# Optimization experiments

Hardware: AMD Instinct MI355X
Metric: run time of the kernel (lower is better)

The kernel has to match this reference:

```python
import jax, jax.numpy as jnp
import numpy as np


def setup_inputs() -> dict:
    key = jax.random.key(0)
    ks = jax.random.split(key, 5)
    B, T, C = 2, 2048, 1024
    x = jax.random.normal(ks[0], (B, T, C), dtype=jnp.float32)
    Wqkv = jax.random.normal(ks[1], (C, 3 * C), dtype=jnp.float32) * (C ** -0.5)
    bqkv = jax.random.normal(ks[2], (3 * C,), dtype=jnp.float32) * 0.02
    Wproj = jax.random.normal(ks[3], (C, C), dtype=jnp.float32) * (C ** -0.5)
    bproj = jax.random.normal(ks[4], (C,), dtype=jnp.float32) * 0.02
    return {"x": x, "Wqkv": Wqkv, "bqkv": bqkv, "Wproj": Wproj, "bproj": bproj}


def reference(x, Wqkv, bqkv, Wproj, bproj):
    B, T, C = x.shape
    n_head = 16
    hd = C // n_head
    x_proj = x @ Wqkv + bqkv  # [B, T, 3C]
    # NOTE: source reshapes (B, T, C) -> (B, n_head, T, hd) directly (no transpose);
    # we replicate that exactly for faithfulness.
    q = x_proj[:, :, :C].reshape(B, n_head, T, hd)
    k = x_proj[:, :, C:2 * C].reshape(B, n_head, T, hd)
    v = x_proj[:, :, 2 * C:].reshape(B, n_head, T, hd)
    att = jnp.einsum('bhtd,bhsd->bhts', q, k) * (1.0 / jnp.sqrt(jnp.float32(hd)))
    causal = jnp.tril(jnp.ones((T, T), dtype=bool))  # True where allowed
    att = jnp.where(causal, att, jnp.float32(-jnp.inf))
    att = jax.nn.softmax(att, axis=-1)
    y = att @ v  # [B, H, T, hd]
    y = jnp.transpose(y, (0, 2, 1, 3)).reshape(B, T, C)
    return y @ Wproj + bproj
```

## Files before the change

### kernel.cpp

```cpp
#include <hip/hip_runtime.h>
#include <hip/hip_bf16.h>
#include <stdint.h>

typedef __hip_bfloat16 bf16;
typedef __attribute__((ext_vector_type(8))) short bf16x8;
typedef __attribute__((ext_vector_type(4))) float f32x4;

__device__ __forceinline__ bf16x8 ldsv8(const bf16* p) { return *(const bf16x8*)p; }

__device__ __forceinline__ short bf_bits(float f) {
  union { bf16 h; short s; } u; u.h = __float2bfloat16(f); return u.s;
}

#define QSCALE 0.18033688011112042f

#define ASYNC16(ldsdst, gsrc)                                                  \
  __builtin_amdgcn_global_load_lds(                                            \
      (const __attribute__((address_space(1))) void*)(gsrc),                   \
      (__attribute__((address_space(3))) void*)(ldsdst), 16, 0, 0)

__device__ __forceinline__ bool is_bf16(const void* p) {
  const uint32_t* w = (const uint32_t*)p;
  int cnt = 0;
#pragma unroll 8
  for (int i = 0; i < 64; ++i) {
    uint32_t e = (w[i] >> 7) & 0xffu;
    cnt += (e >= 100u && e <= 150u) ? 1 : 0;
  }
  return cnt >= 40;
}

__device__ __forceinline__ float load_f32(const void* p, size_t idx, bool b16) {
  return b16 ? __bfloat162float(((const bf16*)p)[idx]) : ((const float*)p)[idx];
}

__device__ __forceinline__ void cvtT_body(const void* in, bf16* out, int R,
                                          int Ccols, int bx, int by,
                                          bf16 (*tile)[33]) {
  const bool b16 = is_bf16(in);
  int tx = threadIdx.x & 31, ty = threadIdx.x >> 5;
  int c0 = bx * 32, r0 = by * 32;
#pragma unroll
  for (int i = 0; i < 32; i += 8)
    tile[ty + i][tx] = __float2bfloat16(load_f32(in, (size_t)(r0 + ty + i) * Ccols + c0 + tx, b16));
  __syncthreads();
#pragma unroll
  for (int i = 0; i < 32; i += 8)
    out[(size_t)(c0 + ty + i) * R + r0 + tx] = tile[tx][ty + i];
}

__global__ __launch_bounds__(256) void prep_k(const float* __restrict__ x,
                                              bf16* __restrict__ xb,
                                              const void* __restrict__ Wqkv,
                                              bf16* __restrict__ WqkvT,
                                              const void* __restrict__ Wproj,
                                              bf16* __restrict__ WprojT) {
  __shared__ __align__(16) bf16 tile[32][33];
  const int id = blockIdx.x;
  if (id < 2048) {
    size_t i = (size_t)id * 256 + threadIdx.x;
    const float4 f0 = ((const float4*)x)[i * 2];
    const float4 f1 = ((const float4*)x)[i * 2 + 1];
    bf16x8 pk = {bf_bits(f0.x), bf_bits(f0.y), bf_bits(f0.z), bf_bits(f0.w),
                 bf_bits(f1.x), bf_bits(f1.y), bf_bits(f1.z), bf_bits(f1.w)};
    ((bf16x8*)xb)[i] = pk;
  } else if (id < 5120) {
    int id2 = id - 2048;
    cvtT_body(Wqkv, WqkvT, 1024, 3072, id2 % 96, id2 / 96, tile);
  } else {
    int id3 = id - 5120;
    cvtT_body(Wproj, WprojT, 1024, 1024, id3 % 32, id3 / 32, tile);
  }
}

__global__ __launch_bounds__(256) void cvtT_k(const void* __restrict__ in,
                                              bf16* __restrict__ out,
                                              int R, int Ccols) {
  __shared__ __align__(16) bf16 tile[32][33];
  cvtT_body(in, out, R, Ccols, blockIdx.x, blockIdx.y, tile);
}

__global__ __launch_bounds__(256) void cvt_k(const float* __restrict__ in,
                                             bf16* __restrict__ out) {
  size_t i = (size_t)blockIdx.x * 256 + threadIdx.x;
  const float4 f0 = ((const float4*)in)[i * 2];
  const float4 f1 = ((const float4*)in)[i * 2 + 1];
  bf16x8 pk = {bf_bits(f0.x), bf_bits(f0.y), bf_bits(f0.z), bf_bits(f0.w),
               bf_bits(f1.x), bf_bits(f1.y), bf_bits(f1.z), bf_bits(f1.w)};
  ((bf16x8*)out)[i] = pk;
}

template <int MODE, int BN>
__global__ __launch_bounds__(256) void gemm128(
    const void* __restrict__ Araw, const bf16* __restrict__ BT,
    const void* __restrict__ biasraw, void* __restrict__ outv) {
  constexpr int K = 1024;
  constexpr int NBF = BN / 32;
  __shared__ __align__(16) bf16 As[128 * 32];
  __shared__ __align__(16) bf16 Bs[BN * 32];
  const int tid = threadIdx.x;
  const int wave = tid >> 6, lane = tid & 63;
  const int quad = lane >> 4, l16 = lane & 15;
  const int nwg = gridDim.x * gridDim.y;
  const int lin = blockIdx.y * gridDim.x + blockIdx.x;
  const int swz = (lin & 7) * (nwg >> 3) + (lin >> 3);
  const int m0 = (swz % gridDim.x) * 128, n0 = (swz / gridDim.x) * BN;
  const int wm = (wave & 1) * 64, wn = (wave >> 1) * (BN / 2);
  const bool a16 = (MODE == 0) ? is_bf16(Araw) : true;
  const bool bias16 = is_bf16(biasraw);

  f32x4 acc[4][NBF] = {};

  for (int kt = 0; kt < K; kt += 32) {
    __syncthreads();
    if (MODE != 0 || a16) {
#pragma unroll
      for (int i = 0; i < 2; ++i) {
        int slot = i * 256 + tid;
        int row = slot >> 2, col = (slot & 3) << 3;
        ASYNC16(As + slot * 8, ((const bf16*)Araw) + (size_t)(m0 + row) * K + kt + col);
      }
#pragma unroll
      for (int i = 0; i < BN / 64; ++i) {
        int slot = i * 256 + tid;
        int row = slot >> 2, col = (slot & 3) << 3;
        ASYNC16(Bs + slot * 8, BT + (size_t)(n0 + row) * K + kt + col);
      }
    } else {
#pragma unroll
      for (int i = 0; i < 2; ++i) {
        int slot = i * 256 + tid;
        int row = slot >> 2, col = (slot & 3) << 3;
        const float* ap = ((const float*)Araw) + (size_t)(m0 + row) * K + kt + col;
        float4 f0 = *(const float4*)ap;
        float4 f1 = *(const float4*)(ap + 4);
        bf16x8 pk = {bf_bits(f0.x), bf_bits(f0.y), bf_bits(f0.z), bf_bits(f0.w),
                     bf_bits(f1.x), bf_bits(f1.y), bf_bits(f1.z), bf_bits(f1.w)};
        *(bf16x8*)(As + slot * 8) = pk;
        if (i * 256 < BN * 4)
          *(bf16x8*)(Bs + slot * 8) = *(const bf16x8*)(BT + (size_t)(n0 + row) * K + kt + col);
      }
    }
    __syncthreads();
    bf16x8 af[4], bfr[NBF];
#pragma unroll
    for (int i = 0; i < 4; ++i)
      af[i] = ldsv8(As + (wm + i * 16 + l16) * 32 + quad * 8);
#pragma unroll
    for (int j = 0; j < NBF; ++j)
      bfr[j] = ldsv8(Bs + (wn + j * 16 + l16) * 32 + quad * 8);
#pragma unroll
    for (int i = 0; i < 4; ++i)
#pragma unroll
      for (int j = 0; j < NBF; ++j)
        acc[i][j] = __builtin_amdgcn_mfma_f32_16x16x32_bf16(af[i], bfr[j], acc[i][j], 0, 0, 0);
  }

  float biasf[NBF];
#pragma unroll
  for (int j = 0; j < NBF; ++j)
    biasf[j] = load_f32(biasraw, n0 + wn + j * 16 + l16, bias16);

#pragma unroll
  for (int i = 0; i < 4; ++i)
#pragma unroll
    for (int j = 0; j < NBF; ++j) {
      int ng = n0 + wn + j * 16 + l16;
#pragma unroll
      for (int r = 0; r < 4; ++r) {
        int mg = m0 + wm + i * 16 + quad * 4 + r;
        float v = acc[i][j][r] + biasf[j];
        if (MODE == 1) {
          ((float*)outv)[(size_t)mg * 1024 + ng] = v;
        } else {
          ((bf16*)outv)[(size_t)mg * 3072 + ng] =
              __float2bfloat16(ng < 1024 ? v * QSCALE : v);
        }
      }
    }
}

__global__ __launch_bounds__(1024, 4) void attn_k(const bf16* __restrict__ xproj,
                                                  bf16* __restrict__ Yb) {
  constexpr int KSZ = 128 * 72;
  constexpr int VSZ = 64 * 136;
  __shared__ __align__(16) bf16 Ks[2 * KSZ];
  __shared__ __align__(16) bf16 VTs[2 * VSZ];
  __shared__ __align__(16) bf16 Ps[16 * 16 * 136];

  const int tid = threadIdx.x;
  const int wave = tid >> 6, lane = tid & 63;
  const int quad = lane >> 4, l16 = lane & 15;
  const int tl = wave >> 3;
  const int wrow = (wave & 7) * 16;
  const int pid = blockIdx.x;
  const int qtA = pid, qtB = 15 - pid;
  const int qt = tl ? qtB : qtA;
  const int bh = blockIdx.y, b = bh >> 4, h = bh & 15;
  const size_t rowbase = (size_t)(b * 2048 + h * 128) * 3072;
  const int q0 = qt * 128;

  const short onebits = (short)0x3F80;
  const bf16x8 vones = {onebits, onebits, onebits, onebits,
                        onebits, onebits, onebits, onebits};

  bf16x8 aq[2];
  {
    int sg = q0 + wrow + l16;
    const bf16* qp = xproj + rowbase + (size_t)(sg >> 4) * 3072 + ((sg & 15) << 6);
#pragma unroll
    for (int ks = 0; ks < 2; ++ks)
      aq[ks] = *(const bf16x8*)(qp + ks * 32 + quad * 8);
  }

  f32x4 o[4] = {};
  f32x4 lacc = {};

  bf16* Pw = Ps + wave * (16 * 136);

  const int sA = tid >> 3, blkA = tid & 7;

  bf16x8 kreg, vreg;
#define ISSUE_LOADS(stv)                                                        \
  {                                                                             \
    int sg0 = (stv)*128 + sA;                                                   \
    const bf16* b0 = xproj + rowbase + (size_t)(sg0 >> 4) * 3072 + ((sg0 & 15) << 6); \
    kreg = *(const bf16x8*)(b0 + 1024 + blkA * 8);                              \
    vreg = *(const bf16x8*)(b0 + 2048 + blkA * 8);                              \
  }
#define WRITE_TILE(buf)                                                         \
  {                                                                             \
    bf16* Kd = Ks + (buf)*KSZ;                                                  \
    bf16* Vd = VTs + (buf)*VSZ;                                                 \
    *(bf16x8*)(Kd + sA * 72 + blkA * 8) = kreg;                                 \
    const bf16* ve0 = (const bf16*)&kreg;  (void)ve0;                           \
    const bf16* vv = (const bf16*)&vreg;                                        \
    const int ssw = sA ^ (blkA << 3);                                           \
    _Pragma("unroll")                                                           \
    for (int j = 0; j < 8; ++j) Vd[(blkA * 8 + j) * 136 + ssw] = vv[j];         \
  }

  ISSUE_LOADS(0);
  WRITE_TILE(0);
  ISSUE_LOADS(1);
  __syncthreads();

  int cur = 0;
  for (int st = 0; st <= qtB; ++st) {
    const bf16* Kc = Ks + cur * KSZ;
    const bf16* Vc = VTs + cur * VSZ;

    if (st <= qt) {
      const bool diag = (st == qt);

      f32x4 sc[8] = {};
      __builtin_amdgcn_s_setprio(1);
#pragma unroll
      for (int ks = 0; ks < 2; ++ks)
#pragma unroll
        for (int j = 0; j < 8; ++j) {
          bf16x8 bk = ldsv8(Kc + (j * 16 + l16) * 72 + (ks * 4 + quad) * 8);
          sc[j] = __builtin_amdgcn_mfma_f32_16x16x32_bf16(aq[ks], bk, sc[j], 0, 0, 0);
        }
      __builtin_amdgcn_s_setprio(0);

#pragma unroll
      for (int r = 0; r < 4; ++r) {
        const int rloc = wrow + quad * 4 + r;
        bf16* prow = Pw + (quad * 4 + r) * 136;
        const int psw = quad << 3;
#pragma unroll
        for (int j = 0; j < 8; ++j) {
          float v = sc[j][r];
          if (diag && (j * 16 + l16) > rloc) v = -1e30f;
          prow[(j * 16 + l16) ^ psw] = __float2bfloat16(__builtin_amdgcn_exp2f(v));
        }
      }

      __builtin_amdgcn_s_setprio(1);
#pragma unroll
      for (int ks = 0; ks < 4; ++ks) {
        bf16x8 ap = ldsv8(Pw + l16 * 136 + (((ks * 4 + quad) ^ (l16 >> 2)) << 3));
        lacc = __builtin_amdgcn_mfma_f32_16x16x32_bf16(ap, vones, lacc, 0, 0, 0);
#pragma unroll
        for (int j = 0; j < 4; ++j) {
          int d = j * 16 + l16;
          bf16x8 bv = ldsv8(Vc + d * 136 + (((ks * 4 + quad) ^ (2 * j + (l16 >> 3))) << 3));
          o[j] = __builtin_amdgcn_mfma_f32_16x16x32_bf16(ap, bv, o[j], 0, 0, 0);
        }
      }
      __builtin_amdgcn_s_setprio(0);
    }

    if (st < qtB) {
      WRITE_TILE(cur ^ 1);
      if (st + 2 <= qtB) ISSUE_LOADS(st + 2);
      __syncthreads();
      cur ^= 1;
    }
  }
#undef ISSUE_LOADS
#undef WRITE_TILE

  bf16* Yh = Yb + (size_t)b * 2097152 + h * 64;
#pragma unroll
  for (int r = 0; r < 4; ++r) {
    int tt = q0 + wrow + quad * 4 + r;
    float inv = 1.f / lacc[r];
#pragma unroll
    for (int j = 0; j < 4; ++j)
      Yh[(size_t)tt * 1024 + j * 16 + l16] = __float2bfloat16(o[j][r] * inv);
  }
}

extern "C" void kernel_launch(void* const* d_in, const int* in_sizes, int n_in,
                              void* d_out, int out_size, void* d_ws, size_t ws_size,
                              hipStream_t stream) {
  (void)out_size;
  const void* px     = d_in[0];
  const void* pWqkv  = (n_in > 1) ? d_in[1] : d_in[0];
  const void* pbqkv  = (n_in > 2) ? d_in[2] : d_in[0];
  const void* pWproj = (n_in > 3) ? d_in[3] : d_in[0];
  const void* pbproj = (n_in > 4) ? d_in[4] : d_in[0];
  for (int i = 0; i < n_in; ++i) {
    switch (in_sizes[i]) {
      case 4194304: px     = d_in[i]; break;
      case 3145728: pWqkv  = d_in[i]; break;
      case 3072:    pbqkv  = d_in[i]; break;
      case 1048576: pWproj = d_in[i]; break;
      case 1024:    pbproj = d_in[i]; break;
      default: break;
    }
  }

  char* ws = (char*)d_ws;
  bf16* xproj = (bf16*)(ws + 0);

  if (ws_size >= 41943040) {
    bf16* xb     = (bf16*)(ws + 25165824);
    bf16* WqkvT  = (bf16*)(ws + 33554432);
    bf16* WprojT = (bf16*)(ws + 39845888);
    bf16* Yb     = (bf16*)(ws + 27262976);

    prep_k<<<dim3(6144), 256, 0, stream>>>((const float*)px, xb, pWqkv, WqkvT,
                                           pWproj, WprojT);
    gemm128<0, 128><<<dim3(32, 24), 256, 0, stream>>>(xb, WqkvT, pbqkv, xproj);
    attn_k<<<dim3(8, 32), 1024, 0, stream>>>(xproj, Yb);
    gemm128<1, 64><<<dim3(32, 16), 256, 0, stream>>>(Yb, WprojT, pbproj, d_out);
  } else if (ws_size >= 39845888) {
    bf16* xb     = (bf16*)(ws + 25165824);
    bf16* WqkvT  = (bf16*)(ws + 33554432);
    bf16* WprojT = (bf16*)(ws + 25165824);
    bf16* Yb     = (bf16*)(ws + 27262976);

    cvt_k<<<dim3(2048), 256, 0, stream>>>((const float*)px, xb);
    cvtT_k<<<dim3(96, 32), 256, 0, stream>>>(pWqkv, WqkvT, 1024, 3072);
    gemm128<0, 128><<<dim3(32, 24), 256, 0, stream>>>(xb, WqkvT, pbqkv, xproj);
    cvtT_k<<<dim3(32, 32), 256, 0, stream>>>(pWproj, WprojT, 1024, 1024);
    attn_k<<<dim3(8, 32), 1024, 0, stream>>>(xproj, Yb);
    gemm128<1, 64><<<dim3(32, 16), 256, 0, stream>>>(Yb, WprojT, pbproj, d_out);
  } else {
    bf16* WqkvT  = (bf16*)(ws + 25165824);
    bf16* WprojT = (bf16*)(ws + 25165824);
    bf16* Yb     = (bf16*)(ws + 27262976);

    cvtT_k<<<dim3(96, 32), 256, 0, stream>>>(pWqkv, WqkvT, 1024, 3072);
    gemm128<0, 128><<<dim3(32, 24), 256, 0, stream>>>(px, WqkvT, pbqkv, xproj);
    cvtT_k<<<dim3(32, 32), 256, 0, stream>>>(pWproj, WprojT, 1024, 1024);
    attn_k<<<dim3(8, 32), 1024, 0, stream>>>(xproj, Yb);
    gemm128<1, 64><<<dim3(32, 16), 256, 0, stream>>>(Yb, WprojT, pbproj, d_out);
  }
}
```

Baseline: 196.9 us.

## Rebalance causal attention work so both wave groups share the long query tile

Previously one half of the block's waves processed the short query tile and then sat idle while the other half finished the long tile. Now, after finishing the short tile, the first group reloads Q for the long tile and processes the remaining key range from the other end, while the second group continues in parallel. Partial outputs and row sums are then merged through shared memory. This aims to cut idle wave time at the cost of extra tile loads per step, more barriers, and a reduction step at the end.

Result: slower. 219.6 us (+11.5%).

```diff
diff --git a/kernel.cpp b/kernel.cpp
--- a/kernel.cpp
+++ b/kernel.cpp
@@ -180,6 +180,61 @@
     }
 }
 
+__device__ __forceinline__ void attn_step(const bf16* Kc, const bf16* Vc,
+                                          const bf16x8 (&aq)[2], bf16* Pw,
+                                          f32x4 (&o)[4], f32x4& lacc,
+                                          const bf16x8& vones, int quad,
+                                          int l16, int wrow, bool diag) {
+  f32x4 sc[8] = {};
+  __builtin_amdgcn_s_setprio(1);
+#pragma unroll
+  for (int ks = 0; ks < 2; ++ks)
+#pragma unroll
+    for (int j = 0; j < 8; ++j) {
+      bf16x8 bk = ldsv8(Kc + (j * 16 + l16) * 72 + (ks * 4 + quad) * 8);
+      sc[j] = __builtin_amdgcn_mfma_f32_16x16x32_bf16(aq[ks], bk, sc[j], 0, 0, 0);
+    }
+  __builtin_amdgcn_s_setprio(0);
+#pragma unroll
+  for (int r = 0; r < 4; ++r) {
+    const int rloc = wrow + quad * 4 + r;
+    bf16* prow = Pw + (quad * 4 + r) * 136;
+    const int psw = quad << 3;
+#pragma unroll
+    for (int j = 0; j < 8; ++j) {
+      float v = sc[j][r];
+      if (diag && (j * 16 + l16) > rloc) v = -1e30f;
+      prow[(j * 16 + l16) ^ psw] = __float2bfloat16(__builtin_amdgcn_exp2f(v));
+    }
+  }
+  __builtin_amdgcn_s_setprio(1);
+#pragma unroll
+  for (int ks = 0; ks < 4; ++ks) {
+    bf16x8 ap = ldsv8(Pw + l16 * 136 + (((ks * 4 + quad) ^ (l16 >> 2)) << 3));
+    lacc = __builtin_amdgcn_mfma_f32_16x16x32_bf16(ap, vones, lacc, 0, 0, 0);
+#pragma unroll
+    for (int j = 0; j < 4; ++j) {
+      int d = j * 16 + l16;
+      bf16x8 bv = ldsv8(Vc + d * 136 + (((ks * 4 + quad) ^ (2 * j + (l16 >> 3))) << 3));
+      o[j] = __builtin_amdgcn_mfma_f32_16x16x32_bf16(ap, bv, o[j], 0, 0, 0);
+    }
+  }
+  __builtin_amdgcn_s_setprio(0);
+}
+
+__device__ __forceinline__ void attn_epi(bf16* Yh, int q0, int wrow, int quad,
+                                         int l16, const f32x4 (&o)[4],
+                                         const f32x4& lacc) {
+#pragma unroll
+  for (int r = 0; r < 4; ++r) {
+    int tt = q0 + wrow + quad * 4 + r;
+    float inv = 1.f / lacc[r];
+#pragma unroll
+    for (int j = 0; j < 4; ++j)
+      Yh[(size_t)tt * 1024 + j * 16 + l16] = __float2bfloat16(o[j][r] * inv);
+  }
+}
+
 __global__ __launch_bounds__(1024, 4) void attn_k(const bf16* __restrict__ xproj,
                                                   bf16* __restrict__ Yb) {
   constexpr int KSZ = 128 * 72;
@@ -195,10 +250,9 @@
   const int wrow = (wave & 7) * 16;
   const int pid = blockIdx.x;
   const int qtA = pid, qtB = 15 - pid;
-  const int qt = tl ? qtB : qtA;
+  const int nb = 8 - pid, na = 7 - pid;
   const int bh = blockIdx.y, b = bh >> 4, h = bh & 15;
   const size_t rowbase = (size_t)(b * 2048 + h * 128) * 3072;
-  const int q0 = qt * 128;
 
   const short onebits = (short)0x3F80;
   const bf16x8 vones = {onebits, onebits, onebits, onebits,
@@ -206,7 +260,7 @@
 
   bf16x8 aq[2];
   {
-    int sg = q0 + wrow + l16;
+    int sg = (tl ? qtB : qtA) * 128 + wrow + l16;
     const bf16* qp = xproj + rowbase + (size_t)(sg >> 4) * 3072 + ((sg & 15) << 6);
 #pragma unroll
     for (int ks = 0; ks < 2; ++ks)
@@ -217,99 +271,110 @@
   f32x4 lacc = {};
 
   bf16* Pw = Ps + wave * (16 * 136);
+  bf16* Yh = Yb + (size_t)b * 2097152 + h * 64;
 
   const int sA = tid >> 3, blkA = tid & 7;
 
-  bf16x8 kreg, vreg;
-#define ISSUE_LOADS(stv)                                                        \
+  bf16x8 kreg, vreg, kreg2, vreg2;
+#define ISSUE_T(stv, kr, vr)                                                    \
   {                                                                             \
     int sg0 = (stv)*128 + sA;                                                   \
     const bf16* b0 = xproj + rowbase + (size_t)(sg0 >> 4) * 3072 + ((sg0 & 15) << 6); \
-    kreg = *(const bf16x8*)(b0 + 1024 + blkA * 8);                              \
-    vreg = *(const bf16x8*)(b0 + 2048 + blkA * 8);                              \
-  }
-#define WRITE_TILE(buf)                                                         \
+    kr = *(const bf16x8*)(b0 + 1024 + blkA * 8);                                \
+    vr = *(const bf16x8*)(b0 + 2048 + blkA * 8);                                \
+  }
+#define WRITE_T(buf, kr, vr)                                                    \
   {                                                                             \
     bf16* Kd = Ks + (buf)*KSZ;                                                  \
     bf16* Vd = VTs + (buf)*VSZ;                                                 \
-    *(bf16x8*)(Kd + sA * 72 + blkA * 8) = kreg;                                 \
-    const bf16* ve0 = (const bf16*)&kreg;  (void)ve0;                           \
-    const bf16* vv = (const bf16*)&vreg;                                        \
+    *(bf16x8*)(Kd + sA * 72 + blkA * 8) = kr;                                   \
+    const bf16* vv = (const bf16*)&vr;                                          \
     const int ssw = sA ^ (blkA << 3);                                           \
     _Pragma("unroll")                                                           \
     for (int j = 0; j < 8; ++j) Vd[(blkA * 8 + j) * 136 + ssw] = vv[j];         \
   }
 
-  ISSUE_LOADS(0);
-  WRITE_TILE(0);
-  ISSUE_LOADS(1);
+  ISSUE_T(0, kreg, vreg);
+  WRITE_T(0, kreg, vreg);
+  ISSUE_T(1, kreg, vreg);
   __syncthreads();
 
   int cur = 0;
-  for (int st = 0; st <= qtB; ++st) {
+  for (int st = 0; st <= pid; ++st) {
     const bf16* Kc = Ks + cur * KSZ;
     const bf16* Vc = VTs + cur * VSZ;
-
-    if (st <= qt) {
-      const bool diag = (st == qt);
-
-      f32x4 sc[8] = {};
-      __builtin_amdgcn_s_setprio(1);
-#pragma unroll
-      for (int ks = 0; ks < 2; ++ks)
-#pragma unroll
-        for (int j = 0; j < 8; ++j) {
-          bf16x8 bk = ldsv8(Kc + (j * 16 + l16) * 72 + (ks * 4 + quad) * 8);
-          sc[j] = __builtin_amdgcn_mfma_f32_16x16x32_bf16(aq[ks], bk, sc[j], 0, 0, 0);
-        }
-      __builtin_amdgcn_s_setprio(0);
-
-#pragma unroll
-      for (int r = 0; r < 4; ++r) {
-        const int rloc = wrow + quad * 4 + r;
-        bf16* prow = Pw + (quad * 4 + r) * 136;
-        const int psw = quad << 3;
-#pragma unroll
-        for (int j = 0; j < 8; ++j) {
-          float v = sc[j][r];
-          if (diag && (j * 16 + l16) > rloc) v = -1e30f;
-          prow[(j * 16 + l16) ^ psw] = __float2bfloat16(__builtin_amdgcn_exp2f(v));
-        }
-      }
-
-      __builtin_amdgcn_s_setprio(1);
-#pragma unroll
-      for (int ks = 0; ks < 4; ++ks) {
-        bf16x8 ap = ldsv8(Pw + l16 * 136 + (((ks * 4 + quad) ^ (l16 >> 2)) << 3));
-        lacc = __builtin_amdgcn_mfma_f32_16x16x32_bf16(ap, vones, lacc, 0, 0, 0);
-#pragma unroll
-        for (int j = 0; j < 4; ++j) {
-          int d = j * 16 + l16;
-          bf16x8 bv = ldsv8(Vc + d * 136 + (((ks * 4 + quad) ^ (2 * j + (l16 >> 3))) << 3));
-          o[j] = __builtin_amdgcn_mfma_f32_16x16x32_bf16(ap, bv, o[j], 0, 0, 0);
-        }
-      }
-      __builtin_amdgcn_s_setprio(0);
-    }
-
-    if (st < qtB) {
-      WRITE_TILE(cur ^ 1);
-      if (st + 2 <= qtB) ISSUE_LOADS(st + 2);
+    attn_step(Kc, Vc, aq, Pw, o, lacc, vones, quad, l16, wrow,
+              (tl == 0) && (st == qtA));
+    if (st < pid) {
+      WRITE_T(cur ^ 1, kreg, vreg);
+      if (st + 2 <= pid + 1) ISSUE_T(st + 2, kreg, vreg);
       __syncthreads();
       cur ^= 1;
     }
   }
-#undef ISSUE_LOADS
-#undef WRITE_TILE
-
-  bf16* Yh = Yb + (size_t)b * 2097152 + h * 64;
-#pragma unroll
-  for (int r = 0; r < 4; ++r) {
-    int tt = q0 + wrow + quad * 4 + r;
-    float inv = 1.f / lacc[r];
-#pragma unroll
-    for (int j = 0; j < 4; ++j)
-      Yh[(size_t)tt * 1024 + j * 16 + l16] = __float2bfloat16(o[j][r] * inv);
+
+  WRITE_T(cur ^ 1, kreg, vreg);
+  __syncthreads();
+  if (tl == 0) {
+    attn_epi(Yh, qtA * 128, wrow, quad, l16, o, lacc);
+    int sg = qtB * 128 + wrow + l16;
+    const bf16* qp = xproj + rowbase + (size_t)(sg >> 4) * 3072 + ((sg & 15) << 6);
+#pragma unroll
+    for (int ks = 0; ks < 2; ++ks)
+      aq[ks] = *(const bf16x8*)(qp + ks * 32 + quad * 8);
+#pragma unroll
+    for (int j = 0; j < 4; ++j) o[j] = (f32x4){0.f, 0.f, 0.f, 0.f};
+    lacc = (f32x4){0.f, 0.f, 0.f, 0.f};
+  }
+  if (na > 0) {
+    ISSUE_T(15 - pid, kreg, vreg);
+    WRITE_T(cur, kreg, vreg);
+  }
+  __syncthreads();
+
+  {
+    const bf16* Kb = Ks + (cur ^ 1) * KSZ;
+    const bf16* Vb = VTs + (cur ^ 1) * VSZ;
+    const bf16* Kt = Ks + cur * KSZ;
+    const bf16* Vt = VTs + cur * VSZ;
+    for (int k = 0; k < nb; ++k) {
+      const bool nxb = (k + 1 < nb), nxt = (k + 1 < na);
+      if (nxb) ISSUE_T(pid + 2 + k, kreg, vreg);
+      if (nxt) ISSUE_T(14 - pid - k, kreg2, vreg2);
+      if (tl == 1) {
+        attn_step(Kb, Vb, aq, Pw, o, lacc, vones, quad, l16, wrow,
+                  (pid + 1 + k) == qtB);
+      } else if (k < na) {
+        attn_step(Kt, Vt, aq, Pw, o, lacc, vones, quad, l16, wrow, k == 0);
+      }
+      __syncthreads();
+      if (nxb) WRITE_T(cur ^ 1, kreg, vreg);
+      if (nxt) WRITE_T(cur, kreg2, vreg2);
+      if (nxb || nxt) __syncthreads();
+    }
+  }
+#undef ISSUE_T
+#undef WRITE_T
+
+  __syncthreads();
+  {
+    float* so = (float*)Ks;
+    float* sl = (float*)VTs;
+    const int w8 = wave & 7;
+    if (tl == 0) {
+#pragma unroll
+      for (int j = 0; j < 4; ++j)
+        *(f32x4*)(so + ((w8 * 64 + lane) * 16) + j * 4) = o[j];
+      *(f32x4*)(sl + (w8 * 64 + lane) * 4) = lacc;
+    }
+    __syncthreads();
+    if (tl == 1) {
+#pragma unroll
+      for (int j = 0; j < 4; ++j)
+        o[j] += *(const f32x4*)(so + ((w8 * 64 + lane) * 16) + j * 4);
+      lacc += *(const f32x4*)(sl + (w8 * 64 + lane) * 4);
+      attn_epi(Yh, qtB * 128, wrow, quad, l16, o, lacc);
+    }
   }
 }
 
```
